# Kernel tuning notes

Hardware: AMD Instinct MI355X
Metric: run time of the kernel (lower is better)

Reference implementation:

```python
import jax, jax.numpy as jnp
import numpy as np

B, L = 16, 256
H, NH, NL = 512, 8, 6
NTOK = 10000
P, K = 4, 9          # parser layers, conv kernel size
DFF = 4 * H


def layernorm(x, s=None, b=None, eps=1e-5):
    m = x.mean(-1, keepdims=True)
    v = ((x - m) ** 2).mean(-1, keepdims=True)
    y = (x - m) * jax.lax.rsqrt(v + eps)
    if s is not None:
        y = y * s + b
    return y


def conv1d(h, w, b):
    # h: (B,L,C); w: (K,Cin,Cout); 'same' padding (K odd)
    pad = (K - 1) // 2
    return jax.lax.conv_general_dilated(
        h, w, (1,), [(pad, pad)], dimension_numbers=('NWC', 'WIO', 'NWC')) + b


def setup_inputs():
    key = jax.random.key(0)
    ks = iter(jax.random.split(key, 40))
    r = lambda shape, s=0.02: jax.random.normal(next(ks), shape, jnp.float32) * s
    return dict(
        x=jax.random.randint(next(ks), (B, L), 0, NTOK, jnp.int32),
        pos=jnp.tile(jnp.arange(L, dtype=jnp.int32), (B, 1)),
        emb=r((NTOK, H), 0.1),
        conv_w=r((P, K, H, H)), conv_b=jnp.zeros((P, H)),
        parent_w=r((H, H)), parent_b=jnp.zeros((H,)),
        child_w=r((H, H)), child_b=jnp.zeros((H,)),
        rel_w_param=r((NL, NH, 2), 0.1),
        qkv_w=r((NL, 3 * H, H)), qkv_b=jnp.zeros((NL, 3 * H)),
        out_w=r((NL, H, H)), out_b=jnp.zeros((NL, H)),
        ln1_s=jnp.ones((NL, H)), ln1_b=jnp.zeros((NL, H)),
        ln2_s=jnp.ones((NL, H)), ln2_b=jnp.zeros((NL, H)),
        ff1_w=r((NL, DFF, H)), ff1_b=jnp.zeros((NL, DFF)),
        ff2_w=r((NL, H, DFF)), ff2_b=jnp.zeros((NL, H)),
        norm_s=jnp.ones((H,)), norm_b=jnp.zeros((H,)),
        out_bias=jnp.zeros((NTOK,)),
    )


def _forward(x, floats):
    (emb, conv_w, conv_b, parent_w, parent_b, child_w, child_b, rel_w_param,
     qkv_w, qkv_b, out_w, out_b, ln1_s, ln1_b, ln2_s, ln2_b,
     ff1_w, ff1_b, ff2_w, ff2_b, norm_s, norm_b, out_bias) = floats
    mask = x != 0  # pad token index = 0
    DH = H // NH
    scale = H ** -0.5
    # ---- differentiable parser: Conv1d + LN(no affine) + Tanh stack ----
    h = emb[x]
    for i in range(P):
        h = jnp.where(mask[..., None], h, 0.0)
        h = jnp.tanh(layernorm(conv1d(h, conv_w[i], conv_b[i])))
    parent = h @ parent_w.T + parent_b
    child = h @ child_w.T + child_b
    logits = jnp.einsum('bid,bjd->bij', child, parent) * scale
    logits = jnp.where(mask[:, None, :], logits, -jnp.inf)
    # NB: source applies scaling twice (masked_fill then softmax(logits*scaling))
    p = jax.nn.softmax(logits * scale, axis=-1)  # (B,L,L) head distribution
    # ---- structural relations -> per-layer/per-head attention bias ----
    eye = jnp.eye(L, dtype=bool)
    head = jnp.where(eye, 0.0, p)
    child_rel = jnp.swapaxes(head, 1, 2)
    rel = jnp.stack([head, child_rel], axis=1)            # (B,2,L,L)
    rel_weight = jax.nn.softmax(rel_w_param, axis=-1)     # (NL,NH,2)
    dep = jnp.einsum('lhr,brij->lbhij', rel_weight, rel)  # (NL,B,NH,L,L)
    # ---- pre-LN transformer encoder with structural bias injection ----
    logvis = jnp.where(mask, 0.0, -jnp.inf)[:, None, None, :]  # key padding mask (log)
    h = emb[x]
    for i in range(NL):
        hn = layernorm(h, ln1_s[i], ln1_b[i])
        qkv = hn @ qkv_w[i].T + qkv_b[i]
        q, k, v = jnp.split(qkv, 3, axis=-1)
        split = lambda t: t.reshape(B, L, NH, DH).transpose(0, 2, 1, 3)
        q, k, v = split(q), split(k), split(v)
        att = jnp.einsum('bhid,bhjd->bhij', q, k) * (DH ** -0.5) + dep[i] + logvis
        att = jax.nn.softmax(att, axis=-1)
        ctx = jnp.einsum('bhij,bhjd->bhid', att, v).transpose(0, 2, 1, 3).reshape(B, L, H)
        h = h + ctx @ out_w[i].T + out_b[i]
        hn = layernorm(h, ln2_s[i], ln2_b[i])
        h = h + jax.nn.leaky_relu(hn @ ff1_w[i].T + ff1_b[i], 0.01) @ ff2_w[i].T + ff2_b[i]
    raw = layernorm(h, norm_s, norm_b)
    out = (raw @ emb.T + out_bias).reshape(B * L, NTOK)  # tied output embedding
    return out


def reference(x, pos, emb, conv_w, conv_b, parent_w, parent_b, child_w, child_b,
              rel_w_param, qkv_w, qkv_b, out_w, out_b, ln1_s, ln1_b, ln2_s, ln2_b,
              ff1_w, ff1_b, ff2_w, ff2_b, norm_s, norm_b, out_bias):
    floats = (emb, conv_w, conv_b, parent_w, parent_b, child_w, child_b, rel_w_param,
              qkv_w, qkv_b, out_w, out_b, ln1_s, ln1_b, ln2_s, ln2_b,
              ff1_w, ff1_b, ff2_w, ff2_b, norm_s, norm_b, out_bias)
    return _forward(x, floats)
```

## Files before the change

kernel.cpp:

```cpp
#include <hip/hip_runtime.h>
#include <hip/hip_bf16.h>


typedef unsigned short u16;
typedef unsigned char  u8;
typedef short short8 __attribute__((ext_vector_type(8)));
typedef float f32x4  __attribute__((ext_vector_type(4)));

static constexpr int CB=16, CL=256, CH=512, CNH=8, CDH=64, CNL=6;
static constexpr int CNTOK=10000, CP=4, CKS=9, CDFF=2048, CT=CB*CL;
static constexpr int NTOKP=10112;
static constexpr int LP=264;

__device__ __forceinline__ u16 f2b(float x){
    union { float f; unsigned u; } v; v.f = x;
    unsigned r = v.u + 0x7fffu + ((v.u >> 16) & 1u);
    return (u16)(r >> 16);
}
__device__ __forceinline__ float b2f(u16 u){
    union { unsigned u; float f; } v; v.u = ((unsigned)u) << 16; return v.f;
}
__device__ __forceinline__ unsigned pack2(float a, float b){
    return (unsigned)f2b(a) | ((unsigned)f2b(b) << 16);
}
__device__ __forceinline__ void gll16(const void* g, void* l){
    __builtin_amdgcn_global_load_lds(
        (__attribute__((address_space(1))) void*)g,
        (__attribute__((address_space(3))) void*)l, 16, 0, 0);
}

__global__ __launch_bounds__(256) void cvt_k(const float* __restrict__ in,
    u16* __restrict__ out, long n, long total)
{
    long i = ((long)blockIdx.x * 256 + threadIdx.x) * 8;
    if (i >= total) return;
    uint4 o;
    if (i < n) {
        float4 a = *(const float4*)(in + i);
        float4 b = *(const float4*)(in + i + 4);
        o.x = pack2(a.x, a.y); o.y = pack2(a.z, a.w);
        o.z = pack2(b.x, b.y); o.w = pack2(b.z, b.w);
    } else { o.x = o.y = o.z = o.w = 0u; }
    *(uint4*)(out + i) = o;
}

__global__ __launch_bounds__(256) void embed2_k(const int* __restrict__ x,
    const float* __restrict__ emb, float* __restrict__ h,
    u16* __restrict__ ppad, u8* __restrict__ maskb)
{
    int t = blockIdx.x, tid = threadIdx.x;
    int tok = x[t];
    bool mk = (tok != 0);
    if (tid == 0) maskb[t] = mk ? 1 : 0;
    const float* e = emb + (size_t)tok * CH;
    float v0 = e[tid], v1 = e[tid + 256];
    float* hp = h + (size_t)t * CH;
    hp[tid] = v0; hp[tid + 256] = v1;
    int pr = (t >> 8) * LP + 4 + (t & 255);
    u16* ap = ppad + (size_t)pr * CH;
    ap[tid]       = mk ? f2b(v0) : (u16)0;
    ap[tid + 256] = mk ? f2b(v1) : (u16)0;
}

template<bool INBF, bool AFFINE, bool DOTANH, int OUTMODE>
__global__ __launch_bounds__(256) void ln_k(const void* __restrict__ in,
    const float* __restrict__ s, const float* __restrict__ b, u16* __restrict__ out,
    const u8* __restrict__ mask)
{
    int t = blockIdx.x, tid = threadIdx.x;
    float x0, x1;
    if (INBF) {
        const u16* row = (const u16*)in + (size_t)t * CH;
        x0 = b2f(row[tid]); x1 = b2f(row[tid + 256]);
    } else {
        const float* row = (const float*)in + (size_t)t * CH;
        x0 = row[tid]; x1 = row[tid + 256];
    }
    float sum = x0 + x1, sq = x0*x0 + x1*x1;
    #pragma unroll
    for (int o = 32; o; o >>= 1) { sum += __shfl_down(sum, o); sq += __shfl_down(sq, o); }
    __shared__ float rs[4], rq[4];
    int w = tid >> 6, lane = tid & 63;
    if (lane == 0) { rs[w] = sum; rq[w] = sq; }
    __syncthreads();
    sum = rs[0] + rs[1] + rs[2] + rs[3];
    sq  = rq[0] + rq[1] + rq[2] + rq[3];
    float mean = sum * (1.f/512.f);
    float var  = fmaxf(sq * (1.f/512.f) - mean*mean, 0.f);
    float rstd = rsqrtf(var + 1e-5f);
    float y0 = (x0 - mean) * rstd, y1 = (x1 - mean) * rstd;
    if (AFFINE) {
        y0 = y0 * s[tid]       + b[tid];
        y1 = y1 * s[tid + 256] + b[tid + 256];
    }
    if (DOTANH) { y0 = tanhf(y0); y1 = tanhf(y1); }
    if (OUTMODE == 0) {
        u16* o = out + (size_t)t * CH;
        o[tid] = f2b(y0); o[tid + 256] = f2b(y1);
    } else {
        bool mk = mask[t] != 0;
        int pr = (t >> 8) * LP + 4 + (t & 255);
        u16* o = out + (size_t)pr * CH;
        o[tid]       = mk ? f2b(y0) : (u16)0;
        o[tid + 256] = mk ? f2b(y1) : (u16)0;
    }
}

__global__ __launch_bounds__(256) void tp_conv(const float* __restrict__ src,
    u16* __restrict__ dst)
{
    __shared__ float tile[32][33];
    int z = blockIdx.z, p = z / 9, t = z % 9;
    int ci0 = blockIdx.y * 32, co0 = blockIdx.x * 32;
    int tx = threadIdx.x, ty = threadIdx.y;
    #pragma unroll
    for (int yy = 0; yy < 4; yy++) {
        int i = ty + yy*8;
        tile[i][tx] = src[((size_t)z*512 + ci0 + i)*512 + co0 + tx];
    }
    __syncthreads();
    #pragma unroll
    for (int yy = 0; yy < 4; yy++) {
        int i = ty + yy*8;
        dst[((size_t)p*512 + co0 + i)*4608 + (size_t)t*512 + ci0 + tx] = f2b(tile[tx][i]);
    }
}

__global__ __launch_bounds__(256) void tp_head(const float* __restrict__ src,
    float* __restrict__ dst)
{
    __shared__ float tile[32][33];
    int b = blockIdx.z;
    int i0 = blockIdx.y * 32, j0 = blockIdx.x * 32;
    int tx = threadIdx.x & 31, ty = threadIdx.x >> 5;
    #pragma unroll
    for (int yy = 0; yy < 4; yy++) {
        int i = ty + yy*8;
        tile[i][tx] = src[((size_t)b*256 + i0 + i)*256 + j0 + tx];
    }
    __syncthreads();
    #pragma unroll
    for (int yy = 0; yy < 4; yy++) {
        int i = ty + yy*8;
        dst[((size_t)b*256 + j0 + i)*256 + i0 + tx] = tile[tx][i];
    }
}

template<int BM, bool CONV, int ACT, int OUT, int SPLITK>
__global__ __launch_bounds__(256) void gemm2(
    const u16* __restrict__ A, const u16* __restrict__ B,
    const float* __restrict__ bias, void* __restrict__ Cv,
    int M, int N, int K, float alpha, long sA, long sB, long sC, int swz)
{
    constexpr int MI = BM / 32;
    __shared__ __align__(16) u16 As[32 * BM];
    __shared__ __align__(16) u16 Bs[4096];

    int bx = blockIdx.x, by = blockIdx.y;
    if (swz) {
        int nwg = gridDim.x * gridDim.y;
        int bid = by * gridDim.x + bx;
        bid = (bid & 7) * (nwg >> 3) + (bid >> 3);
        if (swz == 2) { by = bid % gridDim.y; bx = bid / gridDim.y; }
        else          { bx = bid % gridDim.x; by = bid / gridDim.x; }
    }
    const int tid  = threadIdx.x;
    const int lane = tid & 63, wave = tid >> 6;
    const int q = lane >> 4, ln = lane & 15;
    const int wm = wave >> 1, wn = wave & 1;
    const int m0 = by * BM, n0 = bx * 128;
    const int z  = blockIdx.z;

    int kbeg = 0, kend = K;
    if (SPLITK > 1) {
        int ks = K / SPLITK;
        kbeg = z * ks; kend = kbeg + ks;
    } else {
        A += (size_t)z * sA; B += (size_t)z * sB;
    }

    f32x4 acc[MI][4];
    #pragma unroll
    for (int i = 0; i < MI; i++)
        #pragma unroll
        for (int j = 0; j < 4; j++)
            #pragma unroll
            for (int r = 0; r < 4; r++) acc[i][j][r] = 0.f;

    for (int k0 = kbeg; k0 < kend; k0 += 32) {
        if (CONV) {
            int tap = k0 >> 9;
            int ci  = (k0 & 511) + wave*8;
            int gr  = m0 + lane;
            int pr  = (gr >> 8) * LP + (gr & 255) + tap;
            gll16(A + (size_t)pr * CH + ci, As + wave*512);
        } else if (BM == 128) {
            #pragma unroll
            for (int t = 0; t < 2; t++) {
                int c = wave + t*4;
                int kq = c >> 1, rh = (c & 1) << 6;
                gll16(A + (size_t)(m0 + rh + lane) * K + k0 + kq*8, As + c*512);
            }
        } else {
            gll16(A + (size_t)(m0 + lane) * K + k0 + wave*8, As + wave*512);
        }
        #pragma unroll
        for (int t = 0; t < 2; t++) {
            int c = wave + t*4;
            int kq = c >> 1, rh = (c & 1) << 6;
            gll16(B + (size_t)(n0 + rh + lane) * K + k0 + kq*8, Bs + c*512);
        }
        __syncthreads();
        short8 af[MI], bf[4];
        #pragma unroll
        for (int f = 0; f < MI; f++)
            af[f] = *(const short8*)&As[q*(BM*8) + (wm*(BM/2) + f*16 + ln)*8];
        #pragma unroll
        for (int g = 0; g < 4; g++)
            bf[g] = *(const short8*)&Bs[q*1024 + (wn*64 + g*16 + ln)*8];
        #pragma unroll
        for (int f = 0; f < MI; f++)
            #pragma unroll
            for (int g = 0; g < 4; g++)
                acc[f][g] = __builtin_amdgcn_mfma_f32_16x16x32_bf16(af[f], bf[g], acc[f][g], 0, 0, 0);
        __syncthreads();
    }
    float* Cf = (float*)Cv; u16* Cb = (u16*)Cv;
    size_t zoff = (SPLITK > 1) ? 0 : (size_t)z * sC;
    bool addb = bias && (SPLITK == 1 || z == 0);
    #pragma unroll
    for (int f = 0; f < MI; f++) {
        int row0 = m0 + wm*(BM/2) + f*16 + q*4;
        #pragma unroll
        for (int g = 0; g < 4; g++) {
            int col = n0 + wn*64 + g*16 + ln;
            if (col < N) {
                #pragma unroll
                for (int r = 0; r < 4; r++) {
                    float v = acc[f][g][r] * alpha;
                    if (addb) v += bias[col];
                    if (ACT == 1) v = v > 0.f ? v : 0.01f * v;
                    size_t idx = zoff + (size_t)(row0 + r) * N + col;
                    if (OUT == 0)      Cf[idx] = v;
                    else if (OUT == 1) Cb[idx] = f2b(v);
                    else if (OUT == 2) Cf[idx] += v;
                    else               atomicAdd(&Cf[idx], v);
                }
            }
        }
    }
}

__global__ __launch_bounds__(256) void softmax_head(float* __restrict__ sc,
    const u8* __restrict__ mask)
{
    int bi = blockIdx.x;
    int b = bi >> 8, i = bi & 255;
    int j = threadIdx.x;
    float* rowp = sc + (size_t)bi * CL;
    bool valid = mask[(b << 8) | j] != 0;
    float v = valid ? rowp[j] : -1e30f;
    float mx = v;
    #pragma unroll
    for (int o = 32; o; o >>= 1) mx = fmaxf(mx, __shfl_down(mx, o));
    __shared__ float rm[4], rsum[4];
    int w = j >> 6, lane = j & 63;
    if (lane == 0) rm[w] = mx;
    __syncthreads();
    mx = fmaxf(fmaxf(rm[0], rm[1]), fmaxf(rm[2], rm[3]));
    float e = valid ? __expf(v - mx) : 0.f;
    float ssum = e;
    #pragma unroll
    for (int o = 32; o; o >>= 1) ssum += __shfl_down(ssum, o);
    if (lane == 0) rsum[w] = ssum;
    __syncthreads();
    ssum = rsum[0] + rsum[1] + rsum[2] + rsum[3];
    float r = e / fmaxf(ssum, 1e-30f);
    if (j == i) r = 0.f;
    rowp[j] = r;
}

__global__ __launch_bounds__(256) void attn_k(const u16* __restrict__ qkv,
    const float* __restrict__ head, const float* __restrict__ headT,
    const float* __restrict__ relw, const u8* __restrict__ mask,
    u16* __restrict__ ctx, int layer)
{
    __shared__ __align__(16) u16 Ks[CL * CDH];
    __shared__ __align__(16) u16 Vs[CL * CDH];
    int bx = blockIdx.x;
    int b = bx >> 4, hd = (bx >> 1) & 7, qh = bx & 1;
    int tid = threadIdx.x;

    #pragma unroll
    for (int r = 0; r < 8; r++) {
        int ef = tid + 256 * r;
        int j = ef >> 3, d8 = (ef & 7) * 8;
        const u16* ps = qkv + (size_t)(b*256 + j) * 1536 + 512 + hd*64 + d8;
        *(uint4*)&Ks[j*64 + d8] = *(const uint4*)ps;
        *(uint4*)&Vs[j*64 + d8] = *(const uint4*)(ps + 512);
    }

    int qi = qh * 128 + (tid >> 1);
    int half = tid & 1;
    float qv[CDH];
    {
        const u16* qp = qkv + (size_t)(b*256 + qi) * 1536 + hd*64;
        #pragma unroll
        for (int c = 0; c < 8; c++) {
            uint4 u = *(const uint4*)(qp + c*8);
            unsigned uu[4] = {u.x, u.y, u.z, u.w};
            #pragma unroll
            for (int p2 = 0; p2 < 4; p2++) {
                qv[c*8 + p2*2]     = b2f((u16)(uu[p2] & 0xffffu));
                qv[c*8 + p2*2 + 1] = b2f((u16)(uu[p2] >> 16));
            }
        }
    }
    float r0 = relw[((layer << 3) + hd) * 2 + 0];
    float r1 = relw[((layer << 3) + hd) * 2 + 1];
    float e0 = __expf(r0), e1 = __expf(r1);
    float w0 = e0 / (e0 + e1), w1 = 1.f - w0;

    __syncthreads();

    const float* h1 = head  + ((size_t)b << 16) + ((size_t)qi << 8);
    const float* h2 = headT + ((size_t)b << 16) + ((size_t)qi << 8);
    const u8* mb = mask + (b << 8);

    float m = -1e30f, lsum = 0.f;
    float acc[CDH];
    #pragma unroll
    for (int d = 0; d < CDH; d++) acc[d] = 0.f;

    for (int jj = 0; jj < 128; jj++) {
        int j = half * 128 + jj;
        if (!mb[j]) continue;
        float dot = 0.f;
        #pragma unroll
        for (int d = 0; d < CDH; d++) dot += qv[d] * b2f(Ks[(j << 6) + d]);
        float s = dot * 0.125f + w0 * h1[j] + w1 * h2[j];
        float mn = fmaxf(m, s);
        float c = __expf(m - mn);
        float p = __expf(s - mn);
        lsum = lsum * c + p;
        #pragma unroll
        for (int d = 0; d < CDH; d++) acc[d] = acc[d] * c + p * b2f(Vs[(j << 6) + d]);
        m = mn;
    }
    {
        float mo = __shfl_xor(m, 1);
        float lo = __shfl_xor(lsum, 1);
        float M  = fmaxf(m, mo);
        float cs = __expf(m - M);
        float co = __expf(mo - M);
        lsum = lsum * cs + lo * co;
        #pragma unroll
        for (int d = 0; d < CDH; d++) {
            float ao = __shfl_xor(acc[d], 1);
            acc[d] = acc[d] * cs + ao * co;
        }
    }
    if (half == 0) {
        float inv = 1.f / fmaxf(lsum, 1e-30f);
        u16* cp = ctx + (size_t)(b*256 + qi) * CH + (hd << 6);
        #pragma unroll
        for (int d = 0; d < CDH; d++) cp[d] = f2b(acc[d] * inv);
    }
}

extern "C" void kernel_launch(void* const* d_in, const int* in_sizes, int n_in,
                              void* d_out, int out_size, void* d_ws, size_t ws_size,
                              hipStream_t stream)
{
    const int*   x        = (const int*)d_in[0];
    const float* emb      = (const float*)d_in[2];
    const float* conv_w   = (const float*)d_in[3];
    const float* conv_b   = (const float*)d_in[4];
    const float* parent_w = (const float*)d_in[5];
    const float* parent_b = (const float*)d_in[6];
    const float* child_w  = (const float*)d_in[7];
    const float* child_b  = (const float*)d_in[8];
    const float* rel_w    = (const float*)d_in[9];
    const float* qkv_w    = (const float*)d_in[10];
    const float* qkv_b    = (const float*)d_in[11];
    const float* out_w    = (const float*)d_in[12];
    const float* out_b    = (const float*)d_in[13];
    const float* ln1_s    = (const float*)d_in[14];
    const float* ln1_b    = (const float*)d_in[15];
    const float* ln2_s    = (const float*)d_in[16];
    const float* ln2_b    = (const float*)d_in[17];
    const float* ff1_w    = (const float*)d_in[18];
    const float* ff1_b    = (const float*)d_in[19];
    const float* ff2_w    = (const float*)d_in[20];
    const float* ff2_b    = (const float*)d_in[21];
    const float* norm_s   = (const float*)d_in[22];
    const float* norm_b   = (const float*)d_in[23];
    const float* out_bias = (const float*)d_in[24];

    float* ws = (float*)d_ws;
    float* h      = ws;
    float* headp  = ws + 2097152;
    u16*   abuf   = (u16*)(ws + 3145728);
    u16*   Rb     = (u16*)(ws + 4194304);
    u16*   qkvb   = Rb;
    u16*   ppad   = Rb;
    u16*   parentb= Rb;
    u16*   childb = Rb + 2097152;
    u16*   convo  = Rb + 4194304;
    u16*   ctxb   = (u16*)(ws + 7340032);
    u16*   ff1b   = (u16*)(ws + 8388608);
    u16*   convwb = (u16*)(ws + 7340032);
    u8*    maskb  = (u8*)(ws + 12582912);
    u16*   ebf16  = (u16*)(ws + 12583936);
    u16*   qkvwb  = (u16*)(ws + 15172608);
    u16*   outwb  = (u16*)(ws + 17531904);
    u16*   ff1wb  = (u16*)(ws + 18318336);
    u16*   ff2wb  = (u16*)(ws + 21464064);
    u16*   parwb  = (u16*)(ws + 24609792);
    u16*   chlwb  = (u16*)(ws + 24740864);
    float* headT  = (float*)d_out;

    tp_conv<<<dim3(16,16,36), dim3(32,8), 0, stream>>>(conv_w, convwb);
    cvt_k<<<2528, 256, 0, stream>>>(emb,      ebf16, (long)CNTOK*CH, (long)NTOKP*CH);
    cvt_k<<<2304, 256, 0, stream>>>(qkv_w,    qkvwb, 4718592L, 4718592L);
    cvt_k<<< 768, 256, 0, stream>>>(out_w,    outwb, 1572864L, 1572864L);
    cvt_k<<<3072, 256, 0, stream>>>(ff1_w,    ff1wb, 6291456L, 6291456L);
    cvt_k<<<3072, 256, 0, stream>>>(ff2_w,    ff2wb, 6291456L, 6291456L);
    cvt_k<<< 128, 256, 0, stream>>>(parent_w, parwb,  262144L,  262144L);
    cvt_k<<< 128, 256, 0, stream>>>(child_w,  chlwb,  262144L,  262144L);

    hipMemsetAsync(ppad, 0, (size_t)CB * LP * CH * 2, stream);
    embed2_k<<<CT, 256, 0, stream>>>(x, emb, h, ppad, maskb);
    for (int p = 0; p < CP; p++) {
        gemm2<64,true,0,1,1><<<dim3(4,64,1), 256, 0, stream>>>(
            ppad, convwb + (size_t)p*512*4608, conv_b + p*512, convo,
            CT, 512, 4608, 1.f, 0, 0, 0, 2);
        if (p < CP-1)
            ln_k<true,false,true,1><<<CT, 256, 0, stream>>>(convo, nullptr, nullptr, ppad, maskb);
        else
            ln_k<true,false,true,0><<<CT, 256, 0, stream>>>(convo, nullptr, nullptr, abuf, nullptr);
    }
    gemm2<64,false,0,1,1><<<dim3(4,64,1), 256, 0, stream>>>(
        abuf, parwb, parent_b, parentb, CT, 512, 512, 1.f, 0, 0, 0, 2);
    gemm2<64,false,0,1,1><<<dim3(4,64,1), 256, 0, stream>>>(
        abuf, chlwb, child_b, childb, CT, 512, 512, 1.f, 0, 0, 0, 2);
    gemm2<64,false,0,0,1><<<dim3(2,4,16), 256, 0, stream>>>(
        childb, parentb, nullptr, headp, 256, 256, 512, 1.f/512.f,
        131072, 131072, 65536, 0);
    softmax_head<<<CT, 256, 0, stream>>>(headp, maskb);
    tp_head<<<dim3(8,8,16), 256, 0, stream>>>(headp, headT);

    for (int l = 0; l < CNL; l++) {
        ln_k<false,true,false,0><<<CT, 256, 0, stream>>>(h, ln1_s + l*CH, ln1_b + l*CH, abuf, nullptr);
        gemm2<128,false,0,1,1><<<dim3(12,32,1), 256, 0, stream>>>(
            abuf, qkvwb + (size_t)l*1536*512, qkv_b + l*1536, qkvb,
            CT, 1536, 512, 1.f, 0, 0, 0, 1);
        attn_k<<<256, 256, 0, stream>>>(qkvb, headp, headT, rel_w, maskb, ctxb, l);
        gemm2<64,false,0,3,2><<<dim3(4,64,2), 256, 0, stream>>>(
            ctxb, outwb + (size_t)l*512*512, out_b + l*512, h,
            CT, 512, 512, 1.f, 0, 0, 0, 2);
        ln_k<false,true,false,0><<<CT, 256, 0, stream>>>(h, ln2_s + l*CH, ln2_b + l*CH, abuf, nullptr);
        gemm2<128,false,1,1,1><<<dim3(16,32,1), 256, 0, stream>>>(
            abuf, ff1wb + (size_t)l*2048*512, ff1_b + l*2048, ff1b,
            CT, 2048, 512, 1.f, 0, 0, 0, 1);
        gemm2<64,false,0,3,2><<<dim3(4,64,2), 256, 0, stream>>>(
            ff1b, ff2wb + (size_t)l*512*2048, ff2_b + l*512, h,
            CT, 512, 2048, 1.f, 0, 0, 0, 2);
    }
    ln_k<false,true,false,0><<<CT, 256, 0, stream>>>(h, norm_s, norm_b, abuf, nullptr);
    gemm2<128,false,0,0,1><<<dim3(79,32,1), 256, 0, stream>>>(
        abuf, ebf16, out_bias, d_out, CT, CNTOK, 512, 1.f, 0, 0, 0, 2);
}
```

Baseline: 2.511 ms.

## Double-buffer GEMM LDS loads, split-K conv GEMMs, smaller tiles for QKV/FF1

The GEMM kernel now uses two LDS buffers, issuing the next K-slice's global-to-LDS loads before computing the current one, so memory latency overlaps the MFMA work. The parser conv GEMMs switch to 2-way split-K with atomic fp32 accumulation into a zeroed buffer to raise parallelism, and the LayerNorm that follows now reads that fp32 buffer. The QKV and FF1 GEMMs move from 128-row to 64-row tiles to launch more workgroups. The fp32 embedding copy is moved into its own kernel after the parser because its buffer now aliases the conv output. This costs double LDS per block, extra memsets, atomics and a nondeterministic summation order.

```diff
diff --git a/kernel.cpp b/kernel.cpp
--- a/kernel.cpp
+++ b/kernel.cpp
@@ -44,22 +44,27 @@
     *(uint4*)(out + i) = o;
 }
 
-__global__ __launch_bounds__(256) void embed2_k(const int* __restrict__ x,
-    const float* __restrict__ emb, float* __restrict__ h,
-    u16* __restrict__ ppad, u8* __restrict__ maskb)
+__global__ __launch_bounds__(256) void embed_p(const int* __restrict__ x,
+    const float* __restrict__ emb, u16* __restrict__ ppad, u8* __restrict__ maskb)
 {
     int t = blockIdx.x, tid = threadIdx.x;
     int tok = x[t];
     bool mk = (tok != 0);
     if (tid == 0) maskb[t] = mk ? 1 : 0;
     const float* e = emb + (size_t)tok * CH;
-    float v0 = e[tid], v1 = e[tid + 256];
-    float* hp = h + (size_t)t * CH;
-    hp[tid] = v0; hp[tid + 256] = v1;
     int pr = (t >> 8) * LP + 4 + (t & 255);
     u16* ap = ppad + (size_t)pr * CH;
-    ap[tid]       = mk ? f2b(v0) : (u16)0;
-    ap[tid + 256] = mk ? f2b(v1) : (u16)0;
+    ap[tid]       = mk ? f2b(e[tid])       : (u16)0;
+    ap[tid + 256] = mk ? f2b(e[tid + 256]) : (u16)0;
+}
+
+__global__ __launch_bounds__(256) void embed_h(const int* __restrict__ x,
+    const float* __restrict__ emb, float* __restrict__ h)
+{
+    int t = blockIdx.x, tid = threadIdx.x;
+    const float* e = emb + (size_t)x[t] * CH;
+    float* hp = h + (size_t)t * CH;
+    hp[tid] = e[tid]; hp[tid + 256] = e[tid + 256];
 }
 
 template<bool INBF, bool AFFINE, bool DOTANH, int OUTMODE>
@@ -153,8 +158,8 @@
     int M, int N, int K, float alpha, long sA, long sB, long sC, int swz)
 {
     constexpr int MI = BM / 32;
-    __shared__ __align__(16) u16 As[32 * BM];
-    __shared__ __align__(16) u16 Bs[4096];
+    __shared__ __align__(16) u16 As[2 * 32 * BM];
+    __shared__ __align__(16) u16 Bs[2 * 4096];
 
     int bx = blockIdx.x, by = blockIdx.y;
     if (swz) {
@@ -187,43 +192,52 @@
             #pragma unroll
             for (int r = 0; r < 4; r++) acc[i][j][r] = 0.f;
 
-    for (int k0 = kbeg; k0 < kend; k0 += 32) {
+    auto stage = [&](int buf, int k0) {
+        u16* Ad = As + buf * (32 * BM);
+        u16* Bd = Bs + buf * 4096;
         if (CONV) {
             int tap = k0 >> 9;
             int ci  = (k0 & 511) + wave*8;
             int gr  = m0 + lane;
             int pr  = (gr >> 8) * LP + (gr & 255) + tap;
-            gll16(A + (size_t)pr * CH + ci, As + wave*512);
+            gll16(A + (size_t)pr * CH + ci, Ad + wave*512);
         } else if (BM == 128) {
             #pragma unroll
             for (int t = 0; t < 2; t++) {
-                int c = wave + t*4;
-                int kq = c >> 1, rh = (c & 1) << 6;
-                gll16(A + (size_t)(m0 + rh + lane) * K + k0 + kq*8, As + c*512);
+                int c = wave + t*4, kq = c >> 1, rh = (c & 1) << 6;
+                gll16(A + (size_t)(m0 + rh + lane) * K + k0 + kq*8, Ad + c*512);
             }
         } else {
-            gll16(A + (size_t)(m0 + lane) * K + k0 + wave*8, As + wave*512);
+            gll16(A + (size_t)(m0 + lane) * K + k0 + wave*8, Ad + wave*512);
         }
         #pragma unroll
         for (int t = 0; t < 2; t++) {
-            int c = wave + t*4;
-            int kq = c >> 1, rh = (c & 1) << 6;
-            gll16(B + (size_t)(n0 + rh + lane) * K + k0 + kq*8, Bs + c*512);
+            int c = wave + t*4, kq = c >> 1, rh = (c & 1) << 6;
+            gll16(B + (size_t)(n0 + rh + lane) * K + k0 + kq*8, Bd + c*512);
         }
-        __syncthreads();
-        short8 af[MI], bf[4];
+    };
+
+    stage(0, kbeg);
+    __syncthreads();
+    int cur = 0;
+    for (int k0 = kbeg; k0 < kend; k0 += 32) {
+        if (k0 + 32 < kend) stage(cur ^ 1, k0 + 32);
+        const u16* Ac = As + cur * (32 * BM);
+        const u16* Bc = Bs + cur * 4096;
+        short8 af[MI], bg[4];
         #pragma unroll
         for (int f = 0; f < MI; f++)
-            af[f] = *(const short8*)&As[q*(BM*8) + (wm*(BM/2) + f*16 + ln)*8];
+            af[f] = *(const short8*)&Ac[q*(BM*8) + (wm*(BM/2) + f*16 + ln)*8];
         #pragma unroll
         for (int g = 0; g < 4; g++)
-            bf[g] = *(const short8*)&Bs[q*1024 + (wn*64 + g*16 + ln)*8];
+            bg[g] = *(const short8*)&Bc[q*1024 + (wn*64 + g*16 + ln)*8];
         #pragma unroll
         for (int f = 0; f < MI; f++)
             #pragma unroll
             for (int g = 0; g < 4; g++)
-                acc[f][g] = __builtin_amdgcn_mfma_f32_16x16x32_bf16(af[f], bf[g], acc[f][g], 0, 0, 0);
+                acc[f][g] = __builtin_amdgcn_mfma_f32_16x16x32_bf16(af[f], bg[g], acc[f][g], 0, 0, 0);
         __syncthreads();
+        cur ^= 1;
     }
     float* Cf = (float*)Cv; u16* Cb = (u16*)Cv;
     size_t zoff = (SPLITK > 1) ? 0 : (size_t)z * sC;
@@ -399,6 +413,7 @@
 
     float* ws = (float*)d_ws;
     float* h      = ws;
+    float* convo  = ws;
     float* headp  = ws + 2097152;
     u16*   abuf   = (u16*)(ws + 3145728);
     u16*   Rb     = (u16*)(ws + 4194304);
@@ -406,7 +421,6 @@
     u16*   ppad   = Rb;
     u16*   parentb= Rb;
     u16*   childb = Rb + 2097152;
-    u16*   convo  = Rb + 4194304;
     u16*   ctxb   = (u16*)(ws + 7340032);
     u16*   ff1b   = (u16*)(ws + 8388608);
     u16*   convwb = (u16*)(ws + 7340032);
@@ -430,15 +444,16 @@
     cvt_k<<< 128, 256, 0, stream>>>(child_w,  chlwb,  262144L,  262144L);
 
     hipMemsetAsync(ppad, 0, (size_t)CB * LP * CH * 2, stream);
-    embed2_k<<<CT, 256, 0, stream>>>(x, emb, h, ppad, maskb);
+    embed_p<<<CT, 256, 0, stream>>>(x, emb, ppad, maskb);
     for (int p = 0; p < CP; p++) {
-        gemm2<64,true,0,1,1><<<dim3(4,64,1), 256, 0, stream>>>(
+        hipMemsetAsync(convo, 0, (size_t)CT * CH * 4, stream);
+        gemm2<64,true,0,3,2><<<dim3(4,64,2), 256, 0, stream>>>(
             ppad, convwb + (size_t)p*512*4608, conv_b + p*512, convo,
             CT, 512, 4608, 1.f, 0, 0, 0, 2);
         if (p < CP-1)
-            ln_k<true,false,true,1><<<CT, 256, 0, stream>>>(convo, nullptr, nullptr, ppad, maskb);
+            ln_k<false,false,true,1><<<CT, 256, 0, stream>>>(convo, nullptr, nullptr, ppad, maskb);
         else
-            ln_k<true,false,true,0><<<CT, 256, 0, stream>>>(convo, nullptr, nullptr, abuf, nullptr);
+            ln_k<false,false,true,0><<<CT, 256, 0, stream>>>(convo, nullptr, nullptr, abuf, nullptr);
     }
     gemm2<64,false,0,1,1><<<dim3(4,64,1), 256, 0, stream>>>(
         abuf, parwb, parent_b, parentb, CT, 512, 512, 1.f, 0, 0, 0, 2);
@@ -449,10 +464,11 @@
         131072, 131072, 65536, 0);
     softmax_head<<<CT, 256, 0, stream>>>(headp, maskb);
     tp_head<<<dim3(8,8,16), 256, 0, stream>>>(headp, headT);
+    embed_h<<<CT, 256, 0, stream>>>(x, emb, h);
 
     for (int l = 0; l < CNL; l++) {
         ln_k<false,true,false,0><<<CT, 256, 0, stream>>>(h, ln1_s + l*CH, ln1_b + l*CH, abuf, nullptr);
-        gemm2<128,false,0,1,1><<<dim3(12,32,1), 256, 0, stream>>>(
+        gemm2<64,false,0,1,1><<<dim3(12,64,1), 256, 0, stream>>>(
             abuf, qkvwb + (size_t)l*1536*512, qkv_b + l*1536, qkvb,
             CT, 1536, 512, 1.f, 0, 0, 0, 1);
         attn_k<<<256, 256, 0, stream>>>(qkvb, headp, headT, rel_w, maskb, ctxb, l);
@@ -460,7 +476,7 @@
             ctxb, outwb + (size_t)l*512*512, out_b + l*512, h,
             CT, 512, 512, 1.f, 0, 0, 0, 2);
         ln_k<false,true,false,0><<<CT, 256, 0, stream>>>(h, ln2_s + l*CH, ln2_b + l*CH, abuf, nullptr);
-        gemm2<128,false,1,1,1><<<dim3(16,32,1), 256, 0, stream>>>(
+        gemm2<64,false,1,1,1><<<dim3(16,64,1), 256, 0, stream>>>(
             abuf, ff1wb + (size_t)l*2048*512, ff1_b + l*2048, ff1b,
             CT, 2048, 512, 1.f, 0, 0, 0, 1);
         gemm2<64,false,0,3,2><<<dim3(4,64,2), 256, 0, stream>>>(
```

Measured after the change: 2.379 ms. 5.2% less time.
